# Optimization experiments

Hardware: AMD Instinct MI355X
Metric: run time of the kernel (lower is better)

The kernel has to match this reference:

```python
import jax, jax.numpy as jnp
import numpy as np
from jax import lax


def setup_inputs() -> dict:
    key = jax.random.key(0)
    ks = jax.random.split(key, 6)
    B = 65536
    x = jax.random.normal(ks[0], (B, 784), dtype=jnp.float32)
    conv_w = jax.random.normal(ks[1], (3, 3), dtype=jnp.float32)
    w1 = jax.random.normal(ks[2], (676, 128), dtype=jnp.float32) * 0.05
    b1 = jax.random.normal(ks[3], (128,), dtype=jnp.float32) * 0.05
    w2 = jax.random.normal(ks[4], (128, 10), dtype=jnp.float32) * 0.05
    b2 = jax.random.normal(ks[5], (10,), dtype=jnp.float32) * 0.05
    return {"x": x, "conv_w": conv_w, "w1": w1, "b1": b1, "w2": w2, "b2": b2}


def reference(x, conv_w, w1, b1, w2, b2):
    B = x.shape[0]
    img = x.reshape(B, 1, 28, 28)  # NCHW
    # valid 3x3 cross-correlation (tensordot over patch == cross-correlation)
    conv = lax.conv_general_dilated(
        img, conv_w[None, None], window_strides=(1, 1), padding="VALID",
        dimension_numbers=("NCHW", "OIHW", "NCHW"))  # [B,1,26,26]
    h = conv.reshape(B, 26 * 26)
    h = jax.nn.relu(h @ w1 + b1)
    return h @ w2 + b2
```

## Files before the change

kernel.cpp:

```cpp
#include <hip/hip_runtime.h>

typedef __attribute__((ext_vector_type(4))) float floatx4;
typedef __attribute__((ext_vector_type(8))) short short8;
typedef __attribute__((ext_vector_type(4))) unsigned short ushort4v;
typedef __attribute__((ext_vector_type(8))) unsigned short ushort8v;

__device__ __forceinline__ unsigned short f2bf(float f) {
  unsigned int u = __builtin_bit_cast(unsigned int, f);
  u += 0x7FFFu + ((u >> 16) & 1u);
  return (unsigned short)(u >> 16);
}

#define KTOT 784
#define KP   800
#define N1   128
#define BM   128
#define BK   32
#define LDA  36
#define LDH  132

#define LBAR() do { __builtin_amdgcn_s_waitcnt(0xC07F); __builtin_amdgcn_s_barrier(); } while (0)

__global__ void prep_w1eff(const float* __restrict__ conv_w,
                           const float* __restrict__ w1,
                           unsigned short* __restrict__ Bt) {
  const int n = blockIdx.x;
  float cw[9];
#pragma unroll
  for (int i = 0; i < 9; ++i) cw[i] = conv_w[i];
  for (int q = threadIdx.x; q < KP; q += blockDim.x) {
    float acc = 0.f;
    if (q < KTOT) {
      const int r = q / 28, c = q % 28;
#pragma unroll
      for (int di = 0; di < 3; ++di) {
        const int i2 = r - di;
        if (i2 < 0 || i2 >= 26) continue;
#pragma unroll
        for (int dj = 0; dj < 3; ++dj) {
          const int j2 = c - dj;
          if (j2 < 0 || j2 >= 26) continue;
          acc += cw[di * 3 + dj] * w1[(i2 * 26 + j2) * N1 + n];
        }
      }
    }
    Bt[n * KP + q] = f2bf(acc);
  }
}

__global__ __launch_bounds__(256, 2)
void fused_mlp(const float* __restrict__ x,
               const unsigned short* __restrict__ Bt,
               const float* __restrict__ b1,
               const float* __restrict__ w2,
               const float* __restrict__ b2,
               float* __restrict__ out) {
  __shared__ __align__(16) unsigned short sA[2 * BM * LDA];
  __shared__ __align__(16) unsigned short sB[2 * N1 * LDA];
  __shared__ __align__(16) unsigned short sH[BM * LDH];
  __shared__ __align__(16) unsigned short sW2t[16 * LDH];
  __shared__ float sB1[N1];
  __shared__ float sB2[16];

  const int tid  = threadIdx.x;
  const int wave = tid >> 6;
  const int lane = tid & 63;
  const int wm = wave & 1;
  const int wn = wave >> 1;
  const int lr = lane & 15;
  const int lq = lane >> 4;

  const long row_base = (long)blockIdx.x * BM;
  const float* xblk = x + row_base * KTOT;

  for (int i = tid; i < 16 * N1; i += 256) {
    const int n = i >> 7, k = i & 127;
    sW2t[n * LDH + k] = (n < 10) ? f2bf(w2[k * 10 + n]) : (unsigned short)0;
  }
  if (tid < N1) sB1[tid] = b1[tid];
  if (tid < 10) sB2[tid] = b2[tid];

  const int akp = tid & 7;
  const int arp = tid >> 3;
  const int bkp = tid & 3;
  const int bnp = tid >> 2;

  floatx4 acc[4][4] = {};

  auto load_a = [&](floatx4* pa, int kt) {
    const int k0 = kt * BK;
#pragma unroll
    for (int p = 0; p < 4; ++p) {
      const int row = p * 32 + arp;
      int kk = k0 + akp * 4;
      if (kk >= KTOT) kk = KTOT - 16;
      pa[p] = *(const floatx4*)(xblk + (long)row * KTOT + kk);
    }
  };
  auto load_b = [&](ushort8v* pb, int kt) {
    const int k0 = kt * BK;
#pragma unroll
    for (int p = 0; p < 2; ++p) {
      const int n = p * 64 + bnp;
      pb[p] = *(const ushort8v*)(Bt + n * KP + k0 + bkp * 8);
    }
  };
  auto store_tile = [&](int buf, const floatx4* pa, const ushort8v* pb) {
    unsigned short* A  = sA + buf * (BM * LDA);
    unsigned short* Bs = sB + buf * (N1 * LDA);
#pragma unroll
    for (int p = 0; p < 4; ++p) {
      ushort4v u;
      u[0] = f2bf(pa[p][0]); u[1] = f2bf(pa[p][1]);
      u[2] = f2bf(pa[p][2]); u[3] = f2bf(pa[p][3]);
      *(ushort4v*)&A[(p * 32 + arp) * LDA + akp * 4] = u;
    }
#pragma unroll
    for (int p = 0; p < 2; ++p)
      *(ushort8v*)&Bs[(p * 64 + bnp) * LDA + bkp * 8] = pb[p];
  };
  auto mfma_step = [&](int buf) {
    const unsigned short* A  = sA + buf * (BM * LDA);
    const unsigned short* Bs = sB + buf * (N1 * LDA);
    short8 af[4], bfv[4];
#pragma unroll
    for (int i = 0; i < 4; ++i)
      af[i] = *(const short8*)&A[(wm * 64 + i * 16 + lr) * LDA + lq * 8];
#pragma unroll
    for (int i = 0; i < 4; ++i)
      bfv[i] = *(const short8*)&Bs[(wn * 64 + i * 16 + lr) * LDA + lq * 8];
#pragma unroll
    for (int im = 0; im < 4; ++im)
#pragma unroll
      for (int in = 0; in < 4; ++in)
        acc[im][in] = __builtin_amdgcn_mfma_f32_16x16x32_bf16(
            af[im], bfv[in], acc[im][in], 0, 0, 0);
  };

  floatx4 pa0[4], pa1[4];
  ushort8v pb0[2], pb1[2];
  load_a(pa0, 0);
  load_b(pb0, 0);
  for (int kt = 0; kt < 24; kt += 2) {
    load_a(pa1, kt + 1);
    load_b(pb1, kt + 1);
    store_tile(0, pa0, pb0);
    LBAR();
    mfma_step(0);
    load_a(pa0, kt + 2);
    load_b(pb0, kt + 2);
    store_tile(1, pa1, pb1);
    LBAR();
    mfma_step(1);
  }
  store_tile(0, pa0, pb0);
  LBAR();
  mfma_step(0);

#pragma unroll
  for (int im = 0; im < 4; ++im) {
#pragma unroll
    for (int in = 0; in < 4; ++in) {
      const int col = wn * 64 + in * 16 + lr;
      const float bb = sB1[col];
#pragma unroll
      for (int r = 0; r < 4; ++r) {
        const int row = wm * 64 + im * 16 + lq * 4 + r;
        const float v = acc[im][in][r] + bb;
        sH[row * LDH + col] = f2bf(v > 0.f ? v : 0.f);
      }
    }
  }
  __syncthreads();

  floatx4 o0 = {0.f, 0.f, 0.f, 0.f}, o1 = {0.f, 0.f, 0.f, 0.f};
  const int m0 = wave * 32;
#pragma unroll
  for (int kc = 0; kc < 4; ++kc) {
    const int kof = kc * 32 + lq * 8;
    const short8 wv = *(const short8*)&sW2t[lr * LDH + kof];
    const short8 a0 = *(const short8*)&sH[(m0 + lr) * LDH + kof];
    const short8 a1 = *(const short8*)&sH[(m0 + 16 + lr) * LDH + kof];
    o0 = __builtin_amdgcn_mfma_f32_16x16x32_bf16(a0, wv, o0, 0, 0, 0);
    o1 = __builtin_amdgcn_mfma_f32_16x16x32_bf16(a1, wv, o1, 0, 0, 0);
  }
  if (lr < 10) {
    const float bb = sB2[lr];
#pragma unroll
    for (int r = 0; r < 4; ++r) {
      const long row = row_base + m0 + lq * 4 + r;
      out[row * 10 + lr] = o0[r] + bb;
      out[(row + 16) * 10 + lr] = o1[r] + bb;
    }
  }
}

extern "C" void kernel_launch(void* const* d_in, const int* in_sizes, int n_in,
                              void* d_out, int out_size, void* d_ws, size_t ws_size,
                              hipStream_t stream) {
  const float* x      = (const float*)d_in[0];
  const float* conv_w = (const float*)d_in[1];
  const float* w1     = (const float*)d_in[2];
  const float* b1     = (const float*)d_in[3];
  const float* w2     = (const float*)d_in[4];
  const float* b2     = (const float*)d_in[5];
  float* out = (float*)d_out;

  unsigned short* Bt = (unsigned short*)d_ws;

  prep_w1eff<<<128, 256, 0, stream>>>(conv_w, w1, Bt);
  fused_mlp<<<65536 / BM, 256, 0, stream>>>(x, Bt, b1, w2, b2, out);
}
```

Baseline: 307.1 us.

## Load MFMA operands directly from global memory, dropping LDS staging

The GEMM main loop no longer stages A and B tiles through shared memory with barriers. Each wave loads its own fragments straight from global memory into registers, converting x to bf16 in registers. This removes LDS writes and reads and the per-step barriers. In exchange each A row is fetched by both wn waves and each B row by both wm waves, doubling global/L2 traffic. The strided per-lane row loads may also coalesce poorly.

```diff
diff --git a/kernel.cpp b/kernel.cpp
--- a/kernel.cpp
+++ b/kernel.cpp
@@ -2,7 +2,6 @@
 
 typedef __attribute__((ext_vector_type(4))) float floatx4;
 typedef __attribute__((ext_vector_type(8))) short short8;
-typedef __attribute__((ext_vector_type(4))) unsigned short ushort4v;
 typedef __attribute__((ext_vector_type(8))) unsigned short ushort8v;
 
 __device__ __forceinline__ unsigned short f2bf(float f) {
@@ -16,10 +15,7 @@
 #define N1   128
 #define BM   128
 #define BK   32
-#define LDA  36
 #define LDH  132
-
-#define LBAR() do { __builtin_amdgcn_s_waitcnt(0xC07F); __builtin_amdgcn_s_barrier(); } while (0)
 
 __global__ void prep_w1eff(const float* __restrict__ conv_w,
                            const float* __restrict__ w1,
@@ -55,8 +51,6 @@
                const float* __restrict__ w2,
                const float* __restrict__ b2,
                float* __restrict__ out) {
-  __shared__ __align__(16) unsigned short sA[2 * BM * LDA];
-  __shared__ __align__(16) unsigned short sB[2 * N1 * LDA];
   __shared__ __align__(16) unsigned short sH[BM * LDH];
   __shared__ __align__(16) unsigned short sW2t[16 * LDH];
   __shared__ float sB1[N1];
@@ -80,82 +74,66 @@
   if (tid < N1) sB1[tid] = b1[tid];
   if (tid < 10) sB2[tid] = b2[tid];
 
-  const int akp = tid & 7;
-  const int arp = tid >> 3;
-  const int bkp = tid & 3;
-  const int bnp = tid >> 2;
+  const float* arow[4];
+  const unsigned short* brow[4];
+#pragma unroll
+  for (int i = 0; i < 4; ++i)
+    arow[i] = xblk + (long)(wm * 64 + i * 16 + lr) * KTOT;
+#pragma unroll
+  for (int j = 0; j < 4; ++j)
+    brow[j] = Bt + (long)(wn * 64 + j * 16 + lr) * KP + lq * 8;
 
   floatx4 acc[4][4] = {};
 
-  auto load_a = [&](floatx4* pa, int kt) {
+  auto load_a = [&](floatx4 (&ra)[4][2], int kt) {
+    int kk = kt * BK + lq * 8;
+    if (kk >= KTOT) kk = 0;
+#pragma unroll
+    for (int i = 0; i < 4; ++i) {
+      ra[i][0] = *(const floatx4*)(arow[i] + kk);
+      ra[i][1] = *(const floatx4*)(arow[i] + kk + 4);
+    }
+  };
+  auto load_b = [&](ushort8v (&rb)[4], int kt) {
     const int k0 = kt * BK;
 #pragma unroll
-    for (int p = 0; p < 4; ++p) {
-      const int row = p * 32 + arp;
-      int kk = k0 + akp * 4;
-      if (kk >= KTOT) kk = KTOT - 16;
-      pa[p] = *(const floatx4*)(xblk + (long)row * KTOT + kk);
+    for (int j = 0; j < 4; ++j)
+      rb[j] = *(const ushort8v*)(brow[j] + k0);
+  };
+  auto compute = [&](const floatx4 (&ra)[4][2], const ushort8v (&rb)[4]) {
+    short8 af[4];
+#pragma unroll
+    for (int i = 0; i < 4; ++i) {
+      ushort8v u;
+      u[0] = f2bf(ra[i][0][0]); u[1] = f2bf(ra[i][0][1]);
+      u[2] = f2bf(ra[i][0][2]); u[3] = f2bf(ra[i][0][3]);
+      u[4] = f2bf(ra[i][1][0]); u[5] = f2bf(ra[i][1][1]);
+      u[6] = f2bf(ra[i][1][2]); u[7] = f2bf(ra[i][1][3]);
+      af[i] = __builtin_bit_cast(short8, u);
     }
-  };
-  auto load_b = [&](ushort8v* pb, int kt) {
-    const int k0 = kt * BK;
-#pragma unroll
-    for (int p = 0; p < 2; ++p) {
-      const int n = p * 64 + bnp;
-      pb[p] = *(const ushort8v*)(Bt + n * KP + k0 + bkp * 8);
-    }
-  };
-  auto store_tile = [&](int buf, const floatx4* pa, const ushort8v* pb) {
-    unsigned short* A  = sA + buf * (BM * LDA);
-    unsigned short* Bs = sB + buf * (N1 * LDA);
-#pragma unroll
-    for (int p = 0; p < 4; ++p) {
-      ushort4v u;
-      u[0] = f2bf(pa[p][0]); u[1] = f2bf(pa[p][1]);
-      u[2] = f2bf(pa[p][2]); u[3] = f2bf(pa[p][3]);
-      *(ushort4v*)&A[(p * 32 + arp) * LDA + akp * 4] = u;
-    }
-#pragma unroll
-    for (int p = 0; p < 2; ++p)
-      *(ushort8v*)&Bs[(p * 64 + bnp) * LDA + bkp * 8] = pb[p];
-  };
-  auto mfma_step = [&](int buf) {
-    const unsigned short* A  = sA + buf * (BM * LDA);
-    const unsigned short* Bs = sB + buf * (N1 * LDA);
-    short8 af[4], bfv[4];
-#pragma unroll
-    for (int i = 0; i < 4; ++i)
-      af[i] = *(const short8*)&A[(wm * 64 + i * 16 + lr) * LDA + lq * 8];
-#pragma unroll
-    for (int i = 0; i < 4; ++i)
-      bfv[i] = *(const short8*)&Bs[(wn * 64 + i * 16 + lr) * LDA + lq * 8];
 #pragma unroll
     for (int im = 0; im < 4; ++im)
 #pragma unroll
       for (int in = 0; in < 4; ++in)
         acc[im][in] = __builtin_amdgcn_mfma_f32_16x16x32_bf16(
-            af[im], bfv[in], acc[im][in], 0, 0, 0);
+            af[im], __builtin_bit_cast(short8, rb[in]), acc[im][in], 0, 0, 0);
   };
 
-  floatx4 pa0[4], pa1[4];
-  ushort8v pb0[2], pb1[2];
-  load_a(pa0, 0);
-  load_b(pb0, 0);
+  floatx4 ra0[4][2], ra1[4][2];
+  ushort8v rb0[4], rb1[4];
+  load_a(ra0, 0);
+  load_b(rb0, 0);
   for (int kt = 0; kt < 24; kt += 2) {
-    load_a(pa1, kt + 1);
-    load_b(pb1, kt + 1);
-    store_tile(0, pa0, pb0);
-    LBAR();
-    mfma_step(0);
-    load_a(pa0, kt + 2);
-    load_b(pb0, kt + 2);
-    store_tile(1, pa1, pb1);
-    LBAR();
-    mfma_step(1);
+    load_a(ra1, kt + 1);
+    load_b(rb1, kt + 1);
+    compute(ra0, rb0);
+    load_a(ra0, kt + 2);
+    load_b(rb0, kt + 2);
+    compute(ra1, rb1);
   }
-  store_tile(0, pa0, pb0);
-  LBAR();
-  mfma_step(0);
+  compute(ra0, rb0);
+
+  __syncthreads();
 
 #pragma unroll
   for (int im = 0; im < 4; ++im) {
```

Result: slower. 335.1 us (+9.1%).

## Halve row tile to 64 with two waves and alias H into A/B shared buffer

Applied to the files above, without the earlier changes.

Shrinks the row tile from 128 to 64 and the block from four waves to two, with each wave covering 64 output columns over all 64 rows. The hidden-activation tile now aliases the A/B staging buffer behind an extra barrier, which cuts the block's LDS footprint so more blocks can be resident and the grid doubles. The cost is that each block re-reads the full bf16 weight tile for half as many rows, doubling weight traffic per row. The second-layer code still uses four waves of 32 rows, so with two waves only rows 0-63 are written and that part is consistent.

```diff
diff --git a/kernel.cpp b/kernel.cpp
--- a/kernel.cpp
+++ b/kernel.cpp
@@ -14,7 +14,7 @@
 #define KTOT 784
 #define KP   800
 #define N1   128
-#define BM   128
+#define BM   64
 #define BK   32
 #define LDA  36
 #define LDH  132
@@ -48,32 +48,33 @@
   }
 }
 
-__global__ __launch_bounds__(256, 2)
+__global__ __launch_bounds__(128, 2)
 void fused_mlp(const float* __restrict__ x,
                const unsigned short* __restrict__ Bt,
                const float* __restrict__ b1,
                const float* __restrict__ w2,
                const float* __restrict__ b2,
                float* __restrict__ out) {
-  __shared__ __align__(16) unsigned short sA[2 * BM * LDA];
-  __shared__ __align__(16) unsigned short sB[2 * N1 * LDA];
-  __shared__ __align__(16) unsigned short sH[BM * LDH];
+  __shared__ __align__(16) unsigned short sAB[2 * BM * LDA + 2 * N1 * LDA];
   __shared__ __align__(16) unsigned short sW2t[16 * LDH];
   __shared__ float sB1[N1];
   __shared__ float sB2[16];
 
+  unsigned short* const sA = sAB;
+  unsigned short* const sB = sAB + 2 * BM * LDA;
+  unsigned short* const sH = sAB;
+
   const int tid  = threadIdx.x;
   const int wave = tid >> 6;
   const int lane = tid & 63;
-  const int wm = wave & 1;
-  const int wn = wave >> 1;
+  const int wn = wave;
   const int lr = lane & 15;
   const int lq = lane >> 4;
 
   const long row_base = (long)blockIdx.x * BM;
   const float* xblk = x + row_base * KTOT;
 
-  for (int i = tid; i < 16 * N1; i += 256) {
+  for (int i = tid; i < 16 * N1; i += 128) {
     const int n = i >> 7, k = i & 127;
     sW2t[n * LDH + k] = (n < 10) ? f2bf(w2[k * 10 + n]) : (unsigned short)0;
   }
@@ -89,21 +90,17 @@
 
   auto load_a = [&](floatx4* pa, int kt) {
     const int k0 = kt * BK;
-#pragma unroll
-    for (int p = 0; p < 4; ++p) {
-      const int row = p * 32 + arp;
-      int kk = k0 + akp * 4;
-      if (kk >= KTOT) kk = KTOT - 16;
-      pa[p] = *(const floatx4*)(xblk + (long)row * KTOT + kk);
-    }
+    int kk = k0 + akp * 4;
+    if (kk >= KTOT) kk = KTOT - 16;
+#pragma unroll
+    for (int p = 0; p < 4; ++p)
+      pa[p] = *(const floatx4*)(xblk + (long)(p * 16 + arp) * KTOT + kk);
   };
   auto load_b = [&](ushort8v* pb, int kt) {
     const int k0 = kt * BK;
 #pragma unroll
-    for (int p = 0; p < 2; ++p) {
-      const int n = p * 64 + bnp;
-      pb[p] = *(const ushort8v*)(Bt + n * KP + k0 + bkp * 8);
-    }
+    for (int p = 0; p < 4; ++p)
+      pb[p] = *(const ushort8v*)(Bt + (p * 32 + bnp) * KP + k0 + bkp * 8);
   };
   auto store_tile = [&](int buf, const floatx4* pa, const ushort8v* pb) {
     unsigned short* A  = sA + buf * (BM * LDA);
@@ -113,11 +110,11 @@
       ushort4v u;
       u[0] = f2bf(pa[p][0]); u[1] = f2bf(pa[p][1]);
       u[2] = f2bf(pa[p][2]); u[3] = f2bf(pa[p][3]);
-      *(ushort4v*)&A[(p * 32 + arp) * LDA + akp * 4] = u;
-    }
-#pragma unroll
-    for (int p = 0; p < 2; ++p)
-      *(ushort8v*)&Bs[(p * 64 + bnp) * LDA + bkp * 8] = pb[p];
+      *(ushort4v*)&A[(p * 16 + arp) * LDA + akp * 4] = u;
+    }
+#pragma unroll
+    for (int p = 0; p < 4; ++p)
+      *(ushort8v*)&Bs[(p * 32 + bnp) * LDA + bkp * 8] = pb[p];
   };
   auto mfma_step = [&](int buf) {
     const unsigned short* A  = sA + buf * (BM * LDA);
@@ -125,10 +122,10 @@
     short8 af[4], bfv[4];
 #pragma unroll
     for (int i = 0; i < 4; ++i)
-      af[i] = *(const short8*)&A[(wm * 64 + i * 16 + lr) * LDA + lq * 8];
-#pragma unroll
-    for (int i = 0; i < 4; ++i)
-      bfv[i] = *(const short8*)&Bs[(wn * 64 + i * 16 + lr) * LDA + lq * 8];
+      af[i] = *(const short8*)&A[(i * 16 + lr) * LDA + lq * 8];
+#pragma unroll
+    for (int j = 0; j < 4; ++j)
+      bfv[j] = *(const short8*)&Bs[(wn * 64 + j * 16 + lr) * LDA + lq * 8];
 #pragma unroll
     for (int im = 0; im < 4; ++im)
 #pragma unroll
@@ -138,7 +135,7 @@
   };
 
   floatx4 pa0[4], pa1[4];
-  ushort8v pb0[2], pb1[2];
+  ushort8v pb0[4], pb1[4];
   load_a(pa0, 0);
   load_b(pb0, 0);
   for (int kt = 0; kt < 24; kt += 2) {
@@ -157,6 +154,8 @@
   LBAR();
   mfma_step(0);
 
+  LBAR();
+
 #pragma unroll
   for (int im = 0; im < 4; ++im) {
 #pragma unroll
@@ -165,7 +164,7 @@
       const float bb = sB1[col];
 #pragma unroll
       for (int r = 0; r < 4; ++r) {
-        const int row = wm * 64 + im * 16 + lq * 4 + r;
+        const int row = im * 16 + lq * 4 + r;
         const float v = acc[im][in][r] + bb;
         sH[row * LDH + col] = f2bf(v > 0.f ? v : 0.f);
       }
@@ -209,5 +208,5 @@
   unsigned short* Bt = (unsigned short*)d_ws;
 
   prep_w1eff<<<128, 256, 0, stream>>>(conv_w, w1, Bt);
-  fused_mlp<<<65536 / BM, 256, 0, stream>>>(x, Bt, b1, w2, b2, out);
-}
+  fused_mlp<<<65536 / BM, 128, 0, stream>>>(x, Bt, b1, w2, b2, out);
+}
```

New measurement: 311.9 us. No clear change (+1.5%).
